# Optimization experiments

Measured on AMD Instinct MI355X. Metric: run time of the kernel, lower is better.

## Reference

```python
import jax, jax.numpy as jnp
import numpy as np

B, S = 4, 2048
IN, OUT = 4096, 11008  # LLaMA-7B FFN up-proj


def setup_inputs() -> dict:
    key = jax.random.key(0)
    k1, k2, k3, k4 = jax.random.split(key, 4)
    x = jax.random.normal(k1, (B, S, IN), dtype=jnp.float32)
    # int4 quantized weight values in [-8, 7], then nibble-pack pairs into bytes
    q = jax.random.randint(k2, (OUT, IN), -8, 8, dtype=jnp.int32)
    lo = q[:, 0::2] & 15           # even-index element -> low nibble
    hi = q[:, 1::2] & 15           # odd-index element  -> high nibble
    weight_q = (lo | (hi << 4)).astype(jnp.int32)  # packed bytes, values in [0, 255], shape [OUT, IN//2]
    # per-output-channel absmax scale (positive floats)
    scale = jax.random.uniform(k3, (OUT,), minval=0.005, maxval=0.02, dtype=jnp.float32)
    bias = jax.random.normal(k4, (OUT,), dtype=jnp.float32) * 0.01
    return {"x": x, "weight_q": weight_q, "scale": scale, "bias": bias}


def _unpack_int4(packed):
    # packed: [out, in//2] ints holding byte values in [0,255]
    lo = packed & 15
    hi = (packed >> 4) & 15
    # sign-extend 4-bit nibbles: values >= 8 map to value - 16 (range [-8, 7])
    lo = lo - 16 * (lo >= 8)
    hi = hi - 16 * (hi >= 8)
    # interleave: even indices = lo, odd indices = hi -> [out, in]
    return jnp.stack([lo, hi], axis=-1).reshape(packed.shape[0], packed.shape[1] * 2)


def reference(x, weight_q, scale, bias):
    # on-the-fly dequant: w[o, i] = q[o, i] * scale[o]
    w = _unpack_int4(weight_q).astype(x.dtype) * scale.astype(x.dtype)[:, None]  # [OUT, IN]
    # F.linear(x, w, bias) == x @ w.T + bias
    return jnp.einsum('bsi,oi->bso', x, w) + bias.astype(x.dtype)
```

## Files before the change

### kernel.cpp

```cpp
#include <hip/hip_runtime.h>
#include <hip/hip_bf16.h>

typedef __attribute__((ext_vector_type(4))) float  f32x4;
typedef __attribute__((ext_vector_type(8))) short  bf16x8;
typedef __attribute__((ext_vector_type(4))) int    i32x4;

#define M_DIM 8192
#define N_DIM 11008
#define K_DIM 4096
#define KP    2048

#define A_WS_BYTES ((size_t)M_DIM * K_DIM * 2)
#define B_WS_BYTES ((size_t)N_DIM * K_DIM * 2)
#define WS_NEED    (A_WS_BYTES + B_WS_BYTES)

#define BM 256
#define BN 256
#define BK 32
#define NT (K_DIM / BK)
#define NBUF 4
#define TILE_A_BYTES (BM * BK * 2)
#define BUF_BYTES    (2 * TILE_A_BYTES)

__device__ __forceinline__ short f2bf(float f) {
    return __builtin_bit_cast(short, __float2bfloat16(f));
}

__global__ __launch_bounds__(256)
void cvt_x_kernel(const float* __restrict__ x, short* __restrict__ xb)
{
    const size_t i = ((size_t)blockIdx.x * 256 + threadIdx.x) * 8;
    const f32x4 a = *(const f32x4*)(x + i);
    const f32x4 b = *(const f32x4*)(x + i + 4);
    bf16x8 o;
    #pragma unroll
    for (int j = 0; j < 4; ++j) {
        o[j]     = f2bf(a[j]);
        o[4 + j] = f2bf(b[j]);
    }
    *(bf16x8*)(xb + i) = o;
}

__global__ __launch_bounds__(256)
void dequant_w_kernel(const int* __restrict__ wq, short* __restrict__ wb)
{
    const size_t i = ((size_t)blockIdx.x * 256 + threadIdx.x) * 4;
    const i32x4 v = *(const i32x4*)(wq + i);
    bf16x8 o;
    #pragma unroll
    for (int j = 0; j < 4; ++j) {
        const int q = (v[j] & 0xFF) ^ 0x88;
        o[2 * j]     = f2bf((float)((q & 15) - 8));
        o[2 * j + 1] = f2bf((float)(((q >> 4) & 15) - 8));
    }
    *(bf16x8*)(wb + i * 2) = o;
}

__global__ __launch_bounds__(512, 2)
void gemm256_kernel(const short* __restrict__ A,
                    const short* __restrict__ Bw,
                    const float* __restrict__ scale,
                    const float* __restrict__ bias,
                    float* __restrict__ out)
{
    __shared__ char lds[NBUF * BUF_BYTES];

    const int t    = threadIdx.x;
    const int lane = t & 63;
    const int wv   = t >> 6;
    const int wm   = wv >> 2;
    const int wn   = wv & 3;

    const int nbx = N_DIM / BN;
    const int cpx = (nbx * (M_DIM / BM)) >> 3;
    const int bid = blockIdx.x;
    const int sid = (bid & 7) * cpx + (bid >> 3);
    const int by  = sid / nbx;
    const int bx  = sid - by * nbx;
    const int m0  = by * BM;
    const int n0  = bx * BN;

    const int srow = lane >> 2;
    const int gp   = lane & 3;

    const short* aSrc[2];
    const short* bSrc[2];
    int aDst[2], bDst[2];
    #pragma unroll
    for (int i = 0; i < 2; ++i) {
        const int c   = wv * 2 + i;
        const int row = c * 16 + srow;
        const int g   = gp ^ ((row >> 1) & 3);
        aSrc[i] = A  + (size_t)(m0 + row) * K_DIM + g * 8;
        bSrc[i] = Bw + (size_t)(n0 + row) * K_DIM + g * 8;
        aDst[i] = c * 1024;
        bDst[i] = TILE_A_BYTES + c * 1024;
    }

#define STAGE(kt_) do {                                                                   \
    const int b_  = (kt_) & (NBUF - 1);                                                   \
    const int ko_ = (kt_) * BK;                                                           \
    _Pragma("unroll")                                                                     \
    for (int i_ = 0; i_ < 2; ++i_) {                                                      \
        __builtin_amdgcn_global_load_lds(                                                 \
            (const __attribute__((address_space(1))) unsigned int*)(aSrc[i_] + ko_),      \
            (__attribute__((address_space(3))) unsigned int*)(lds + b_ * BUF_BYTES + aDst[i_]), \
            16, 0, 0);                                                                    \
        __builtin_amdgcn_global_load_lds(                                                 \
            (const __attribute__((address_space(1))) unsigned int*)(bSrc[i_] + ko_),      \
            (__attribute__((address_space(3))) unsigned int*)(lds + b_ * BUF_BYTES + bDst[i_]), \
            16, 0, 0);                                                                    \
    }                                                                                     \
} while (0)

    const int lr = lane & 15;
    const int lk = lane >> 4;
    int aRd[8], bRd[4];
    #pragma unroll
    for (int mi = 0; mi < 8; ++mi) {
        const int row = wm * 128 + mi * 16 + lr;
        aRd[mi] = row * 64 + ((lk * 16) ^ (((row >> 1) & 3) << 4));
    }
    #pragma unroll
    for (int ni = 0; ni < 4; ++ni) {
        const int row = wn * 64 + ni * 16 + lr;
        bRd[ni] = TILE_A_BYTES + row * 64 + ((lk * 16) ^ (((row >> 1) & 3) << 4));
    }

    f32x4 acc[8][4];
    #pragma unroll
    for (int mi = 0; mi < 8; ++mi)
        #pragma unroll
        for (int ni = 0; ni < 4; ++ni)
            acc[mi][ni] = (f32x4){0.f, 0.f, 0.f, 0.f};

    STAGE(0); STAGE(1); STAGE(2);
    asm volatile("s_waitcnt vmcnt(8)" ::: "memory");
    __builtin_amdgcn_s_barrier();

    for (int kt = 0; kt < NT; ++kt) {
        const char* buf = lds + (kt & (NBUF - 1)) * BUF_BYTES;
        if (kt + 3 < NT) STAGE(kt + 3);

        bf16x8 af[8], bfr[4];
        #pragma unroll
        for (int mi = 0; mi < 8; ++mi) af[mi] = *(const bf16x8*)(buf + aRd[mi]);
        #pragma unroll
        for (int ni = 0; ni < 4; ++ni) bfr[ni] = *(const bf16x8*)(buf + bRd[ni]);

        __builtin_amdgcn_s_setprio(1);
        #pragma unroll
        for (int mi = 0; mi < 8; ++mi)
            #pragma unroll
            for (int ni = 0; ni < 4; ++ni)
                acc[mi][ni] = __builtin_amdgcn_mfma_f32_16x16x32_bf16(
                    af[mi], bfr[ni], acc[mi][ni], 0, 0, 0);
        __builtin_amdgcn_s_setprio(0);

        if (kt < NT - 3)       asm volatile("s_waitcnt vmcnt(8)" ::: "memory");
        else if (kt == NT - 3) asm volatile("s_waitcnt vmcnt(4)" ::: "memory");
        else if (kt == NT - 2) asm volatile("s_waitcnt vmcnt(0)" ::: "memory");
        if (kt < NT - 1) __builtin_amdgcn_s_barrier();
    }

    #pragma unroll
    for (int ni = 0; ni < 4; ++ni) {
        const int gn = n0 + wn * 64 + ni * 16 + lr;
        const float sc = scale[gn];
        const float bi = bias[gn];
        #pragma unroll
        for (int mi = 0; mi < 8; ++mi) {
            const int gm = m0 + wm * 128 + mi * 16 + lk * 4;
            const f32x4 v = acc[mi][ni];
            #pragma unroll
            for (int r = 0; r < 4; ++r)
                out[(size_t)(gm + r) * N_DIM + gn] = v[r] * sc + bi;
        }
    }
#undef STAGE
}

__device__ __forceinline__ int swz(int row, int kbyte) {
    return row * 128 + (kbyte ^ ((row & 7) << 4));
}

__global__ __launch_bounds__(256, 2)
void qlin_kernel(const float* __restrict__ x,
                 const int*   __restrict__ wq,
                 const float* __restrict__ scale,
                 const float* __restrict__ bias,
                 float* __restrict__ out)
{
    __shared__ short As[128 * 64];
    __shared__ short Bs[128 * 64];

    const int t  = threadIdx.x;
    const int n0 = blockIdx.x * 128;
    const int m0 = blockIdx.y * 128;

    const int sr = t >> 1;
    const int sh = t & 1;

    const float* ag = x  + (size_t)(m0 + sr) * K_DIM + sh * 32;
    const int*   bg = wq + (size_t)(n0 + sr) * KP    + sh * 16;

    const int lane = t & 63;
    const int wv   = t >> 6;
    const int wm   = wv >> 1;
    const int wn   = wv & 1;
    const int lr   = lane & 15;
    const int lk   = lane >> 4;

    f32x4 acc[4][4];
    #pragma unroll
    for (int i = 0; i < 4; ++i)
        #pragma unroll
        for (int j = 0; j < 4; ++j)
            acc[i][j] = (f32x4){0.f, 0.f, 0.f, 0.f};

    f32x4 ar[8];
    i32x4 br[4];

    #pragma unroll
    for (int i = 0; i < 8; ++i) ar[i] = *(const f32x4*)(ag + i * 4);
    #pragma unroll
    for (int i = 0; i < 4; ++i) br[i] = *(const i32x4*)(bg + i * 4);

    for (int kt = 0; kt < 64; ++kt) {
        #pragma unroll
        for (int c = 0; c < 4; ++c) {
            bf16x8 pa;
            #pragma unroll
            for (int j = 0; j < 8; ++j)
                pa[j] = f2bf(ar[c * 2 + (j >> 2)][j & 3]);
            *(bf16x8*)((char*)As + swz(sr, sh * 64 + c * 16)) = pa;

            bf16x8 pb;
            #pragma unroll
            for (int j = 0; j < 4; ++j) {
                const int q = br[c][j] ^ 0x88;
                const float flo = __builtin_bit_cast(float, 0x4B000000 | (q & 15))        - 8388616.0f;
                const float fhi = __builtin_bit_cast(float, 0x4B000000 | ((q >> 4) & 15)) - 8388616.0f;
                pb[2 * j]     = f2bf(flo);
                pb[2 * j + 1] = f2bf(fhi);
            }
            *(bf16x8*)((char*)Bs + swz(sr, sh * 64 + c * 16)) = pb;
        }
        __syncthreads();

        if (kt + 1 < 64) {
            const float* an = ag + (kt + 1) * 64;
            const int*   bn = bg + (kt + 1) * 32;
            #pragma unroll
            for (int i = 0; i < 8; ++i) ar[i] = *(const f32x4*)(an + i * 4);
            #pragma unroll
            for (int i = 0; i < 4; ++i) br[i] = *(const i32x4*)(bn + i * 4);
        }

        #pragma unroll
        for (int ks = 0; ks < 2; ++ks) {
            const int kb = ks * 64 + lk * 16;
            bf16x8 af[4], bfr[4];
            #pragma unroll
            for (int mi = 0; mi < 4; ++mi)
                af[mi] = *(const bf16x8*)((const char*)As + swz(wm * 64 + mi * 16 + lr, kb));
            #pragma unroll
            for (int ni = 0; ni < 4; ++ni)
                bfr[ni] = *(const bf16x8*)((const char*)Bs + swz(wn * 64 + ni * 16 + lr, kb));
            #pragma unroll
            for (int mi = 0; mi < 4; ++mi)
                #pragma unroll
                for (int ni = 0; ni < 4; ++ni)
                    acc[mi][ni] = __builtin_amdgcn_mfma_f32_16x16x32_bf16(
                        af[mi], bfr[ni], acc[mi][ni], 0, 0, 0);
        }
        __syncthreads();
    }

    #pragma unroll
    for (int ni = 0; ni < 4; ++ni) {
        const int gn = n0 + wn * 64 + ni * 16 + lr;
        const float sc = scale[gn];
        const float bi = bias[gn];
        #pragma unroll
        for (int mi = 0; mi < 4; ++mi) {
            const int gm = m0 + wm * 64 + mi * 16 + lk * 4;
            const f32x4 v = acc[mi][ni];
            #pragma unroll
            for (int r2 = 0; r2 < 4; ++r2)
                out[(size_t)(gm + r2) * N_DIM + gn] = v[r2] * sc + bi;
        }
    }
}

extern "C" void kernel_launch(void* const* d_in, const int* in_sizes, int n_in,
                              void* d_out, int out_size, void* d_ws, size_t ws_size,
                              hipStream_t stream)
{
    const float* x     = (const float*)d_in[0];
    const int*   wq    = (const int*)d_in[1];
    const float* scale = (const float*)d_in[2];
    const float* bias  = (const float*)d_in[3];
    float*       out   = (float*)d_out;

    if (ws_size >= WS_NEED) {
        short* xb = (short*)d_ws;
        short* wb = (short*)((char*)d_ws + A_WS_BYTES);
        cvt_x_kernel<<<16384, 256, 0, stream>>>(x, xb);
        dequant_w_kernel<<<22016, 256, 0, stream>>>(wq, wb);
        const int nwg = (N_DIM / BN) * (M_DIM / BM);
        gemm256_kernel<<<nwg, 512, 0, stream>>>(xb, wb, scale, bias, out);
    } else {
        qlin_kernel<<<dim3(N_DIM / 128, M_DIM / 128), 256, 0, stream>>>(x, wq, scale, bias, out);
    }
}
```

Measured before the change: 810.9 us.

## Split GEMM main loop into two phases interleaving A/B staging with MFMA halves

Splits the per-k-tile global-to-LDS staging into separate A and B loads and splits the MFMA block into two halves. Each half issues its LDS fragment reads and one half of the next prefetch, then runs its MFMAs, with extra barriers between phases. The goal is to spread memory issue across the compute so loads and MFMAs overlap better, in the style of ping-pong scheduling. The cost is three more workgroup barriers per k iteration, and the vmcnt accounting has to stay correct with the reordered loads.

```diff
diff --git a/kernel.cpp b/kernel.cpp
--- a/kernel.cpp
+++ b/kernel.cpp
@@ -97,20 +97,26 @@
         bDst[i] = TILE_A_BYTES + c * 1024;
     }
 
-#define STAGE(kt_) do {                                                                   \
+#define STAGE_A(kt_) do {                                                                 \
     const int b_  = (kt_) & (NBUF - 1);                                                   \
     const int ko_ = (kt_) * BK;                                                           \
     _Pragma("unroll")                                                                     \
-    for (int i_ = 0; i_ < 2; ++i_) {                                                      \
+    for (int i_ = 0; i_ < 2; ++i_)                                                        \
         __builtin_amdgcn_global_load_lds(                                                 \
             (const __attribute__((address_space(1))) unsigned int*)(aSrc[i_] + ko_),      \
             (__attribute__((address_space(3))) unsigned int*)(lds + b_ * BUF_BYTES + aDst[i_]), \
             16, 0, 0);                                                                    \
+} while (0)
+
+#define STAGE_B(kt_) do {                                                                 \
+    const int b_  = (kt_) & (NBUF - 1);                                                   \
+    const int ko_ = (kt_) * BK;                                                           \
+    _Pragma("unroll")                                                                     \
+    for (int i_ = 0; i_ < 2; ++i_)                                                        \
         __builtin_amdgcn_global_load_lds(                                                 \
             (const __attribute__((address_space(1))) unsigned int*)(bSrc[i_] + ko_),      \
             (__attribute__((address_space(3))) unsigned int*)(lds + b_ * BUF_BYTES + bDst[i_]), \
             16, 0, 0);                                                                    \
-    }                                                                                     \
 } while (0)
 
     const int lr = lane & 15;
@@ -134,27 +140,45 @@
         for (int ni = 0; ni < 4; ++ni)
             acc[mi][ni] = (f32x4){0.f, 0.f, 0.f, 0.f};
 
-    STAGE(0); STAGE(1); STAGE(2);
+    STAGE_A(0); STAGE_B(0);
+    STAGE_A(1); STAGE_B(1);
+    STAGE_A(2); STAGE_B(2);
     asm volatile("s_waitcnt vmcnt(8)" ::: "memory");
     __builtin_amdgcn_s_barrier();
 
     for (int kt = 0; kt < NT; ++kt) {
         const char* buf = lds + (kt & (NBUF - 1)) * BUF_BYTES;
-        if (kt + 3 < NT) STAGE(kt + 3);
-
-        bf16x8 af[8], bfr[4];
-        #pragma unroll
-        for (int mi = 0; mi < 8; ++mi) af[mi] = *(const bf16x8*)(buf + aRd[mi]);
+        bf16x8 af0[4], af1[4], bfr[4];
+
+        #pragma unroll
+        for (int mi = 0; mi < 4; ++mi) af0[mi] = *(const bf16x8*)(buf + aRd[mi]);
         #pragma unroll
         for (int ni = 0; ni < 4; ++ni) bfr[ni] = *(const bf16x8*)(buf + bRd[ni]);
-
+        if (kt + 3 < NT) STAGE_A(kt + 3);
+        __builtin_amdgcn_s_barrier();
+        asm volatile("s_waitcnt lgkmcnt(0)" ::: "memory");
         __builtin_amdgcn_s_setprio(1);
         #pragma unroll
-        for (int mi = 0; mi < 8; ++mi)
+        for (int mi = 0; mi < 4; ++mi)
             #pragma unroll
             for (int ni = 0; ni < 4; ++ni)
                 acc[mi][ni] = __builtin_amdgcn_mfma_f32_16x16x32_bf16(
-                    af[mi], bfr[ni], acc[mi][ni], 0, 0, 0);
+                    af0[mi], bfr[ni], acc[mi][ni], 0, 0, 0);
+        __builtin_amdgcn_s_setprio(0);
+        __builtin_amdgcn_s_barrier();
+
+        #pragma unroll
+        for (int mi = 0; mi < 4; ++mi) af1[mi] = *(const bf16x8*)(buf + aRd[4 + mi]);
+        if (kt + 3 < NT) STAGE_B(kt + 3);
+        __builtin_amdgcn_s_barrier();
+        asm volatile("s_waitcnt lgkmcnt(0)" ::: "memory");
+        __builtin_amdgcn_s_setprio(1);
+        #pragma unroll
+        for (int mi = 0; mi < 4; ++mi)
+            #pragma unroll
+            for (int ni = 0; ni < 4; ++ni)
+                acc[4 + mi][ni] = __builtin_amdgcn_mfma_f32_16x16x32_bf16(
+                    af1[mi], bfr[ni], acc[4 + mi][ni], 0, 0, 0);
         __builtin_amdgcn_s_setprio(0);
 
         if (kt < NT - 3)       asm volatile("s_waitcnt vmcnt(8)" ::: "memory");
@@ -177,7 +201,8 @@
                 out[(size_t)(gm + r) * N_DIM + gn] = v[r] * sc + bi;
         }
     }
-#undef STAGE
+#undef STAGE_A
+#undef STAGE_B
 }
 
 __device__ __forceinline__ int swz(int row, int kbyte) {
```

New measurement: 821.9 us. No clear change (+1.3%).

## Restructure bf16 GEMM main loop into BK=64 double-buffered quadrant-interleaved pipeline

Applied to the files above, without the earlier changes.

Replaces the 4-deep BK=32 prefetch ring with two 64KB LDS buffers at BK=64. Each K-step is split into four quadrant MFMA phases that interleave LDS fragment reads and half-tile global_load_lds issues, with barriers and waitcnts in between. The LDS swizzle is changed to a 128-byte row XOR pattern. The aim is to overlap global loads and LDS reads with MFMA work at a finer grain and to issue fewer, larger stages. The cost is many more barriers per K-step, and the 128KB of LDS may limit occupancy to one block per CU despite launch_bounds(512,2).

```diff
diff --git a/kernel.cpp b/kernel.cpp
--- a/kernel.cpp
+++ b/kernel.cpp
@@ -16,11 +16,12 @@
 
 #define BM 256
 #define BN 256
-#define BK 32
-#define NT (K_DIM / BK)
-#define NBUF 4
-#define TILE_A_BYTES (BM * BK * 2)
-#define BUF_BYTES    (2 * TILE_A_BYTES)
+#define BK 64
+#define NT  (K_DIM / BK)
+#define NIT (NT / 2)
+#define HALF_BYTES 16384
+#define ABUF_BYTES 32768
+#define BUF_BYTES  65536
 
 __device__ __forceinline__ short f2bf(float f) {
     return __builtin_bit_cast(short, __float2bfloat16(f));
@@ -63,7 +64,7 @@
                     const float* __restrict__ bias,
                     float* __restrict__ out)
 {
-    __shared__ char lds[NBUF * BUF_BYTES];
+    __shared__ char lds[2 * BUF_BYTES];
 
     const int t    = threadIdx.x;
     const int lane = t & 63;
@@ -80,51 +81,34 @@
     const int m0  = by * BM;
     const int n0  = bx * BN;
 
-    const int srow = lane >> 2;
-    const int gp   = lane & 3;
-
-    const short* aSrc[2];
-    const short* bSrc[2];
-    int aDst[2], bDst[2];
-    #pragma unroll
-    for (int i = 0; i < 2; ++i) {
-        const int c   = wv * 2 + i;
-        const int row = c * 16 + srow;
-        const int g   = gp ^ ((row >> 1) & 3);
-        aSrc[i] = A  + (size_t)(m0 + row) * K_DIM + g * 8;
-        bSrc[i] = Bw + (size_t)(n0 + row) * K_DIM + g * 8;
-        aDst[i] = c * 1024;
-        bDst[i] = TILE_A_BYTES + c * 1024;
-    }
-
-#define STAGE(kt_) do {                                                                   \
-    const int b_  = (kt_) & (NBUF - 1);                                                   \
-    const int ko_ = (kt_) * BK;                                                           \
-    _Pragma("unroll")                                                                     \
-    for (int i_ = 0; i_ < 2; ++i_) {                                                      \
-        __builtin_amdgcn_global_load_lds(                                                 \
-            (const __attribute__((address_space(1))) unsigned int*)(aSrc[i_] + ko_),      \
-            (__attribute__((address_space(3))) unsigned int*)(lds + b_ * BUF_BYTES + aDst[i_]), \
-            16, 0, 0);                                                                    \
-        __builtin_amdgcn_global_load_lds(                                                 \
-            (const __attribute__((address_space(1))) unsigned int*)(bSrc[i_] + ko_),      \
-            (__attribute__((address_space(3))) unsigned int*)(lds + b_ * BUF_BYTES + bDst[i_]), \
-            16, 0, 0);                                                                    \
-    }                                                                                     \
+    const int srow = t >> 3;
+    const int scol = ((t & 7) ^ (srow & 7)) * 8;
+    const short* aS = A  + (size_t)(m0 + srow) * K_DIM + scol;
+    const short* bS = Bw + (size_t)(n0 + srow) * K_DIM + scol;
+
+#define STG(SRC, MOFF, BUFI, H, KOFF) do {                                                  \
+    _Pragma("unroll")                                                                       \
+    for (int i_ = 0; i_ < 2; ++i_)                                                          \
+        __builtin_amdgcn_global_load_lds(                                                   \
+            (const __attribute__((address_space(1))) unsigned int*)                         \
+                ((SRC) + ((H) * 128 + i_ * 64) * (size_t)K_DIM + (KOFF)),                   \
+            (__attribute__((address_space(3))) unsigned int*)                               \
+                (lds + (BUFI) * BUF_BYTES + (MOFF) + (H) * HALF_BYTES + i_ * 8192 + t * 16),\
+            16, 0, 0);                                                                      \
 } while (0)
 
     const int lr = lane & 15;
     const int lk = lane >> 4;
-    int aRd[8], bRd[4];
+    int aOff[8], bOff[4];
     #pragma unroll
     for (int mi = 0; mi < 8; ++mi) {
         const int row = wm * 128 + mi * 16 + lr;
-        aRd[mi] = row * 64 + ((lk * 16) ^ (((row >> 1) & 3) << 4));
+        aOff[mi] = row * 128 + ((lk ^ (row & 7)) * 16);
     }
     #pragma unroll
     for (int ni = 0; ni < 4; ++ni) {
         const int row = wn * 64 + ni * 16 + lr;
-        bRd[ni] = TILE_A_BYTES + row * 64 + ((lk * 16) ^ (((row >> 1) & 3) << 4));
+        bOff[ni] = ABUF_BYTES + row * 128 + ((lk ^ (row & 7)) * 16);
     }
 
     f32x4 acc[8][4];
@@ -134,33 +118,87 @@
         for (int ni = 0; ni < 4; ++ni)
             acc[mi][ni] = (f32x4){0.f, 0.f, 0.f, 0.f};
 
-    STAGE(0); STAGE(1); STAGE(2);
-    asm volatile("s_waitcnt vmcnt(8)" ::: "memory");
-    __builtin_amdgcn_s_barrier();
-
-    for (int kt = 0; kt < NT; ++kt) {
-        const char* buf = lds + (kt & (NBUF - 1)) * BUF_BYTES;
-        if (kt + 3 < NT) STAGE(kt + 3);
-
-        bf16x8 af[8], bfr[4];
-        #pragma unroll
-        for (int mi = 0; mi < 8; ++mi) af[mi] = *(const bf16x8*)(buf + aRd[mi]);
-        #pragma unroll
-        for (int ni = 0; ni < 4; ++ni) bfr[ni] = *(const bf16x8*)(buf + bRd[ni]);
-
-        __builtin_amdgcn_s_setprio(1);
-        #pragma unroll
-        for (int mi = 0; mi < 8; ++mi)
-            #pragma unroll
-            for (int ni = 0; ni < 4; ++ni)
-                acc[mi][ni] = __builtin_amdgcn_mfma_f32_16x16x32_bf16(
-                    af[mi], bfr[ni], acc[mi][ni], 0, 0, 0);
-        __builtin_amdgcn_s_setprio(0);
-
-        if (kt < NT - 3)       asm volatile("s_waitcnt vmcnt(8)" ::: "memory");
-        else if (kt == NT - 3) asm volatile("s_waitcnt vmcnt(4)" ::: "memory");
-        else if (kt == NT - 2) asm volatile("s_waitcnt vmcnt(0)" ::: "memory");
-        if (kt < NT - 1) __builtin_amdgcn_s_barrier();
+    bf16x8 af[4][2], bf[4][2];
+
+#define RDA(BUFP, MIBASE) do {                                                   \
+    _Pragma("unroll")                                                            \
+    for (int m_ = 0; m_ < 4; ++m_) {                                             \
+        af[m_][0] = *(const bf16x8*)((BUFP) + aOff[(MIBASE) + m_]);              \
+        af[m_][1] = *(const bf16x8*)((BUFP) + (aOff[(MIBASE) + m_] ^ 64));       \
+    }                                                                            \
+} while (0)
+
+#define RDB(BUFP, NIBASE) do {                                                   \
+    _Pragma("unroll")                                                            \
+    for (int n_ = 0; n_ < 2; ++n_) {                                             \
+        bf[(NIBASE) + n_][0] = *(const bf16x8*)((BUFP) + bOff[(NIBASE) + n_]);   \
+        bf[(NIBASE) + n_][1] = *(const bf16x8*)((BUFP) + (bOff[(NIBASE) + n_] ^ 64)); \
+    }                                                                            \
+} while (0)
+
+#define MFMAQ(ACCMI, NIBASE) do {                                                \
+    __builtin_amdgcn_s_setprio(1);                                               \
+    _Pragma("unroll")                                                            \
+    for (int m_ = 0; m_ < 4; ++m_)                                               \
+        _Pragma("unroll")                                                        \
+        for (int n_ = 0; n_ < 2; ++n_) {                                         \
+            acc[(ACCMI) + m_][(NIBASE) + n_] = __builtin_amdgcn_mfma_f32_16x16x32_bf16( \
+                af[m_][0], bf[(NIBASE) + n_][0], acc[(ACCMI) + m_][(NIBASE) + n_], 0, 0, 0); \
+            acc[(ACCMI) + m_][(NIBASE) + n_] = __builtin_amdgcn_mfma_f32_16x16x32_bf16( \
+                af[m_][1], bf[(NIBASE) + n_][1], acc[(ACCMI) + m_][(NIBASE) + n_], 0, 0, 0); \
+        }                                                                        \
+    __builtin_amdgcn_s_setprio(0);                                               \
+} while (0)
+
+#define BAR   __builtin_amdgcn_s_barrier()
+#define LGKM0 asm volatile("s_waitcnt lgkmcnt(0)" ::: "memory")
+#define VMC(N) asm volatile("s_waitcnt vmcnt(" #N ")" ::: "memory")
+
+    STG(bS, ABUF_BYTES, 0, 0, 0);
+    STG(bS, ABUF_BYTES, 0, 1, 0);
+    STG(aS, 0,          0, 0, 0);
+    STG(aS, 0,          0, 1, 0);
+    STG(bS, ABUF_BYTES, 1, 0, BK);
+    STG(bS, ABUF_BYTES, 1, 1, BK);
+    VMC(4);
+    BAR;
+
+    const char* b0p = lds;
+    const char* b1p = lds + BUF_BYTES;
+
+    for (int it = 0; it < NIT; ++it) {
+        const int kc1 = (2 * it + 1) * BK;
+        const int kn0 = (2 * it + 2) * BK;
+        const int kn1 = (2 * it + 3) * BK;
+        const bool nl = (it + 1 < NIT);
+
+        RDA(b0p, 0); RDB(b0p, 0);
+        STG(aS, 0, 1, 0, kc1);
+        BAR; LGKM0; MFMAQ(0, 0); BAR;
+        RDB(b0p, 2);
+        STG(aS, 0, 1, 1, kc1);
+        BAR; LGKM0; MFMAQ(0, 2); BAR;
+        RDA(b0p, 4);
+        if (nl) STG(bS, ABUF_BYTES, 0, 0, kn0);
+        BAR; LGKM0; MFMAQ(4, 2); BAR;
+        if (nl) STG(bS, ABUF_BYTES, 0, 1, kn0);
+        BAR; MFMAQ(4, 0);
+        if (nl) VMC(4); else VMC(0);
+        BAR;
+
+        RDA(b1p, 0); RDB(b1p, 0);
+        if (nl) STG(aS, 0, 0, 0, kn0);
+        BAR; LGKM0; MFMAQ(0, 0); BAR;
+        RDB(b1p, 2);
+        if (nl) STG(aS, 0, 0, 1, kn0);
+        BAR; LGKM0; MFMAQ(0, 2); BAR;
+        RDA(b1p, 4);
+        if (nl) STG(bS, ABUF_BYTES, 1, 0, kn1);
+        BAR; LGKM0; MFMAQ(4, 2); BAR;
+        if (nl) STG(bS, ABUF_BYTES, 1, 1, kn1);
+        BAR; MFMAQ(4, 0);
+        VMC(4);
+        if (nl) BAR;
     }
 
     #pragma unroll
@@ -177,7 +215,13 @@
                 out[(size_t)(gm + r) * N_DIM + gn] = v[r] * sc + bi;
         }
     }
-#undef STAGE
+#undef STG
+#undef RDA
+#undef RDB
+#undef MFMAQ
+#undef BAR
+#undef LGKM0
+#undef VMC
 }
 
 __device__ __forceinline__ int swz(int row, int kbyte) {
@@ -260,19 +304,19 @@
         #pragma unroll
         for (int ks = 0; ks < 2; ++ks) {
             const int kb = ks * 64 + lk * 16;
-            bf16x8 af[4], bfr[4];
+            bf16x8 af2[4], bf2[4];
             #pragma unroll
             for (int mi = 0; mi < 4; ++mi)
-                af[mi] = *(const bf16x8*)((const char*)As + swz(wm * 64 + mi * 16 + lr, kb));
+                af2[mi] = *(const bf16x8*)((const char*)As + swz(wm * 64 + mi * 16 + lr, kb));
             #pragma unroll
             for (int ni = 0; ni < 4; ++ni)
-                bfr[ni] = *(const bf16x8*)((const char*)Bs + swz(wn * 64 + ni * 16 + lr, kb));
+                bf2[ni] = *(const bf16x8*)((const char*)Bs + swz(wn * 64 + ni * 16 + lr, kb));
             #pragma unroll
             for (int mi = 0; mi < 4; ++mi)
                 #pragma unroll
                 for (int ni = 0; ni < 4; ++ni)
                     acc[mi][ni] = __builtin_amdgcn_mfma_f32_16x16x32_bf16(
-                        af[mi], bfr[ni], acc[mi][ni], 0, 0, 0);
+                        af2[mi], bf2[ni], acc[mi][ni], 0, 0, 0);
         }
         __syncthreads();
     }
```

Result: faster. 734.2 us (median of 3 runs) (-9.5%).

## Stream B operand directly into registers and double BK for A-only LDS staging

Applied to the files above, without the earlier changes.

The GEMM main loop now stages only the A tile through LDS, with a 4-deep ring, BK of 64 and an XOR swizzle. B fragments are loaded straight from global memory into double-buffered registers one k-step ahead. The loop is unrolled by four and the MFMAs are grouped into clusters that interleave LDS reads with matrix ops. This removes the LDS traffic and bank pressure for B and halves the number of barriers per K. In exchange it raises register pressure, leaves B global loads uncoalesced across rows, and drops explicit vmcnt waits between stages, which risks races or stalls.

```diff
diff --git a/kernel.cpp b/kernel.cpp
--- a/kernel.cpp
+++ b/kernel.cpp
@@ -16,11 +16,9 @@
 
 #define BM 256
 #define BN 256
-#define BK 32
+#define BK 64
 #define NT (K_DIM / BK)
-#define NBUF 4
-#define TILE_A_BYTES (BM * BK * 2)
-#define BUF_BYTES    (2 * TILE_A_BYTES)
+#define ATILE_BYTES 32768
 
 __device__ __forceinline__ short f2bf(float f) {
     return __builtin_bit_cast(short, __float2bfloat16(f));
@@ -63,7 +61,7 @@
                     const float* __restrict__ bias,
                     float* __restrict__ out)
 {
-    __shared__ char lds[NBUF * BUF_BYTES];
+    __shared__ char lds[4 * ATILE_BYTES];
 
     const int t    = threadIdx.x;
     const int lane = t & 63;
@@ -80,52 +78,45 @@
     const int m0  = by * BM;
     const int n0  = bx * BN;
 
-    const int srow = lane >> 2;
-    const int gp   = lane & 3;
-
-    const short* aSrc[2];
-    const short* bSrc[2];
-    int aDst[2], bDst[2];
-    #pragma unroll
-    for (int i = 0; i < 2; ++i) {
-        const int c   = wv * 2 + i;
-        const int row = c * 16 + srow;
-        const int g   = gp ^ ((row >> 1) & 3);
-        aSrc[i] = A  + (size_t)(m0 + row) * K_DIM + g * 8;
-        bSrc[i] = Bw + (size_t)(n0 + row) * K_DIM + g * 8;
-        aDst[i] = c * 1024;
-        bDst[i] = TILE_A_BYTES + c * 1024;
-    }
-
-#define STAGE(kt_) do {                                                                   \
-    const int b_  = (kt_) & (NBUF - 1);                                                   \
-    const int ko_ = (kt_) * BK;                                                           \
-    _Pragma("unroll")                                                                     \
-    for (int i_ = 0; i_ < 2; ++i_) {                                                      \
-        __builtin_amdgcn_global_load_lds(                                                 \
-            (const __attribute__((address_space(1))) unsigned int*)(aSrc[i_] + ko_),      \
-            (__attribute__((address_space(3))) unsigned int*)(lds + b_ * BUF_BYTES + aDst[i_]), \
-            16, 0, 0);                                                                    \
-        __builtin_amdgcn_global_load_lds(                                                 \
-            (const __attribute__((address_space(1))) unsigned int*)(bSrc[i_] + ko_),      \
-            (__attribute__((address_space(3))) unsigned int*)(lds + b_ * BUF_BYTES + bDst[i_]), \
-            16, 0, 0);                                                                    \
-    }                                                                                     \
+    const int srow = t >> 3;
+    const int scol = ((t & 7) ^ (srow & 7)) * 8;
+    const short* aS = A + (size_t)(m0 + srow) * K_DIM + scol;
+
+#define STAGE_A(kt_) do {                                                               \
+    const int b_ = (kt_) & 3;                                                           \
+    _Pragma("unroll")                                                                   \
+    for (int i_ = 0; i_ < 4; ++i_)                                                      \
+        __builtin_amdgcn_global_load_lds(                                               \
+            (const __attribute__((address_space(1))) unsigned int*)                     \
+                (aS + (size_t)(i_ * 64) * K_DIM + (kt_) * BK),                          \
+            (__attribute__((address_space(3))) unsigned int*)                           \
+                (lds + b_ * ATILE_BYTES + i_ * 8192 + t * 16),                          \
+            16, 0, 0);                                                                  \
 } while (0)
 
     const int lr = lane & 15;
     const int lk = lane >> 4;
-    int aRd[8], bRd[4];
+    int aOff[8];
     #pragma unroll
     for (int mi = 0; mi < 8; ++mi) {
         const int row = wm * 128 + mi * 16 + lr;
-        aRd[mi] = row * 64 + ((lk * 16) ^ (((row >> 1) & 3) << 4));
-    }
-    #pragma unroll
-    for (int ni = 0; ni < 4; ++ni) {
-        const int row = wn * 64 + ni * 16 + lr;
-        bRd[ni] = TILE_A_BYTES + row * 64 + ((lk * 16) ^ (((row >> 1) & 3) << 4));
-    }
+        aOff[mi] = row * 128 + ((lk ^ (row & 7)) * 16);
+    }
+
+    const short* bgl[4];
+    #pragma unroll
+    for (int ni = 0; ni < 4; ++ni)
+        bgl[ni] = Bw + (size_t)(n0 + wn * 64 + ni * 16 + lr) * K_DIM + lk * 8;
+
+    bf16x8 breg[2][4][2];
+
+#define LOADB(P, kt_) do {                                                              \
+    _Pragma("unroll")                                                                   \
+    for (int n_ = 0; n_ < 4; ++n_)                                                      \
+        _Pragma("unroll")                                                               \
+        for (int k_ = 0; k_ < 2; ++k_)                                                  \
+            breg[P][n_][k_] = *(const bf16x8*)(bgl[n_] + (kt_) * BK + k_ * 32);         \
+} while (0)
 
     f32x4 acc[8][4];
     #pragma unroll
@@ -134,33 +125,39 @@
         for (int ni = 0; ni < 4; ++ni)
             acc[mi][ni] = (f32x4){0.f, 0.f, 0.f, 0.f};
 
-    STAGE(0); STAGE(1); STAGE(2);
-    asm volatile("s_waitcnt vmcnt(8)" ::: "memory");
+#define QCLUST(BUFP, MIBASE, KS, P) do {                                                \
+    bf16x8 af_[4];                                                                      \
+    _Pragma("unroll")                                                                   \
+    for (int m_ = 0; m_ < 4; ++m_)                                                      \
+        af_[m_] = *(const bf16x8*)((BUFP) + (aOff[(MIBASE) + m_] ^ ((KS) * 64)));       \
+    __builtin_amdgcn_s_setprio(1);                                                      \
+    _Pragma("unroll")                                                                   \
+    for (int m_ = 0; m_ < 4; ++m_)                                                      \
+        _Pragma("unroll")                                                               \
+        for (int n_ = 0; n_ < 4; ++n_)                                                  \
+            acc[(MIBASE) + m_][n_] = __builtin_amdgcn_mfma_f32_16x16x32_bf16(           \
+                af_[m_], breg[P][n_][KS], acc[(MIBASE) + m_][n_], 0, 0, 0);             \
+    __builtin_amdgcn_s_setprio(0);                                                      \
+} while (0)
+
+    STAGE_A(0); STAGE_A(1); STAGE_A(2);
+    LOADB(0, 0);
+    asm volatile("s_waitcnt vmcnt(16)" ::: "memory");
     __builtin_amdgcn_s_barrier();
 
-    for (int kt = 0; kt < NT; ++kt) {
-        const char* buf = lds + (kt & (NBUF - 1)) * BUF_BYTES;
-        if (kt + 3 < NT) STAGE(kt + 3);
-
-        bf16x8 af[8], bfr[4];
-        #pragma unroll
-        for (int mi = 0; mi < 8; ++mi) af[mi] = *(const bf16x8*)(buf + aRd[mi]);
-        #pragma unroll
-        for (int ni = 0; ni < 4; ++ni) bfr[ni] = *(const bf16x8*)(buf + bRd[ni]);
-
-        __builtin_amdgcn_s_setprio(1);
-        #pragma unroll
-        for (int mi = 0; mi < 8; ++mi)
-            #pragma unroll
-            for (int ni = 0; ni < 4; ++ni)
-                acc[mi][ni] = __builtin_amdgcn_mfma_f32_16x16x32_bf16(
-                    af[mi], bfr[ni], acc[mi][ni], 0, 0, 0);
-        __builtin_amdgcn_s_setprio(0);
-
-        if (kt < NT - 3)       asm volatile("s_waitcnt vmcnt(8)" ::: "memory");
-        else if (kt == NT - 3) asm volatile("s_waitcnt vmcnt(4)" ::: "memory");
-        else if (kt == NT - 2) asm volatile("s_waitcnt vmcnt(0)" ::: "memory");
-        if (kt < NT - 1) __builtin_amdgcn_s_barrier();
+    for (int kt0 = 0; kt0 < NT; kt0 += 4) {
+        #pragma unroll
+        for (int u = 0; u < 4; ++u) {
+            const int kt = kt0 + u;
+            const char* buf = lds + u * ATILE_BYTES;
+            if (kt + 3 < NT) STAGE_A(kt + 3);
+            if (kt + 1 < NT) LOADB((u + 1) & 1, kt + 1);
+            QCLUST(buf, 0, 0, u & 1);
+            QCLUST(buf, 0, 1, u & 1);
+            QCLUST(buf, 4, 0, u & 1);
+            QCLUST(buf, 4, 1, u & 1);
+            __builtin_amdgcn_s_barrier();
+        }
     }
 
     #pragma unroll
@@ -177,7 +174,9 @@
                 out[(size_t)(gm + r) * N_DIM + gn] = v[r] * sc + bi;
         }
     }
-#undef STAGE
+#undef STAGE_A
+#undef LOADB
+#undef QCLUST
 }
 
 __device__ __forceinline__ int swz(int row, int kbyte) {
@@ -260,19 +259,19 @@
         #pragma unroll
         for (int ks = 0; ks < 2; ++ks) {
             const int kb = ks * 64 + lk * 16;
-            bf16x8 af[4], bfr[4];
+            bf16x8 af2[4], bf2[4];
             #pragma unroll
             for (int mi = 0; mi < 4; ++mi)
-                af[mi] = *(const bf16x8*)((const char*)As + swz(wm * 64 + mi * 16 + lr, kb));
+                af2[mi] = *(const bf16x8*)((const char*)As + swz(wm * 64 + mi * 16 + lr, kb));
             #pragma unroll
             for (int ni = 0; ni < 4; ++ni)
-                bfr[ni] = *(const bf16x8*)((const char*)Bs + swz(wn * 64 + ni * 16 + lr, kb));
+                bf2[ni] = *(const bf16x8*)((const char*)Bs + swz(wn * 64 + ni * 16 + lr, kb));
             #pragma unroll
             for (int mi = 0; mi < 4; ++mi)
                 #pragma unroll
                 for (int ni = 0; ni < 4; ++ni)
                     acc[mi][ni] = __builtin_amdgcn_mfma_f32_16x16x32_bf16(
-                        af[mi], bfr[ni], acc[mi][ni], 0, 0, 0);
+                        af2[mi], bf2[ni], acc[mi][ni], 0, 0, 0);
         }
         __syncthreads();
     }
```

After: 1.287 ms. 1.59x slower.
